# Performance work log

Measured on AMD Instinct MI355X. Metric: run time of the kernel, lower is better.

## Reference

```python
import jax, jax.numpy as jnp
import numpy as np

# __init__ constants
COORS_RANGE = ((-51.2, 51.2), (-51.2, 51.2), (-4.0, 2.4))  # x, y, z ranges
SPATIAL = (512, 512, 64)  # base spatial shape (X, Y, Z)
SCALES = (2, 4, 8, 1)     # scale_list + [1]
N_POINTS = 2_000_000
N_BATCH = 8


def setup_inputs() -> dict:
    key = jax.random.key(0)
    kp, kb = jax.random.split(key)
    lo = jnp.array([r[0] for r in COORS_RANGE], dtype=jnp.float32)
    hi = jnp.array([r[1] for r in COORS_RANGE], dtype=jnp.float32)
    u = jax.random.uniform(kp, (N_POINTS, 3), dtype=jnp.float32)
    points = lo + u * (hi - lo)  # [N,3] xyz inside the voxelization range
    batch_idx = jax.random.randint(kb, (N_POINTS,), 0, N_BATCH).astype(jnp.int64)
    return {"points": points, "batch_idx": batch_idx}


def reference(points, batch_idx):
    """Per scale: quantize xyz to voxel indices, then unique/dedup with inverse and
    counts. Rows [b,x,y,z] are packed into a single int64 key so that a 1-D unique
    (lexicographically equivalent to torch.unique(dim=0)) can be used.
    Returns, for each scale in SCALES: (full_coors [N,4] int64, coors_inv [N] int,
    coors [M,4] int32 in [b,z,y,x] order), flattened into one tuple."""
    b = batch_idx.astype(jnp.int64)
    outs = []
    for scale in SCALES:
        dims = [int(np.ceil(s / scale)) for s in SPATIAL]  # per-scale grid size
        idxs = []
        for i in range(3):
            lo, hi = COORS_RANGE[i]
            # torch .long() truncates toward zero; values are >=0 in range so
            # truncation == floor here.
            idxs.append((dims[i] * (points[:, i] - lo) / (hi - lo)).astype(jnp.int64))
        xidx, yidx, zidx = idxs
        full_coors = jnp.stack([b, xidx, yidx, zidx], axis=-1)  # [N,4]
        sx, sy, sz = dims
        # pack (b,x,y,z) lexicographically into one key
        keys = ((b * sx + xidx) * sy + yidx) * sz + zidx
        unq, unq_inv, unq_cnt = jnp.unique(keys, return_inverse=True, return_counts=True)
        zb = unq % sz
        rem = unq // sz
        yb = rem % sy
        rem = rem // sy
        xb = rem % sx
        bb = rem // sx
        # original reorders unq columns to [b, z, y, x] and casts to int32
        coors = jnp.stack([bb, zb, yb, xb], axis=-1).astype(jnp.int32)
        outs.extend([full_coors, unq_inv.reshape(-1), coors])
    return tuple(outs)
```

## Files before the change

kernel.cpp:

```cpp
#include <hip/hip_runtime.h>
#include <stdint.h>


#define CHUNK 4096
#define NB    1174
#define TOTALW 4808704
#define R_S2 0
#define R_S4 528384
#define R_S8 598016
#define R_S1 610304
#define PAD0 524288
#define PAD1 593920
#define PAD2 606208
#define PAD3 4804608
#define NBUCKET 512
#define BCAP 5120
#define KEYBLOCKS 1024
#define ROUND 2048
#define KPT 8

__device__ __forceinline__ uint32_t cmp2(uint32_t w) {
  w = (w | (w >> 1)) & 0x55555555u;
  w = (w | (w >> 1)) & 0x33333333u;
  w = (w | (w >> 2)) & 0x0F0F0F0Fu;
  w = (w | (w >> 4)) & 0x00FF00FFu;
  w = (w | (w >> 8)) & 0x0000FFFFu;
  return w;
}

__global__ __launch_bounds__(256) void k_key(
    const float* __restrict__ pts, const int* __restrict__ bidx, int n,
    uint32_t* __restrict__ keys,
    uint32_t* __restrict__ bucketCount, uint32_t* __restrict__ bucketData,
    uint32_t* __restrict__ chunkSums) {
  __shared__ uint32_t cnt[NBUCKET], inc[NBUCKET], pos[NBUCKET], gpos[NBUCKET];
  __shared__ uint32_t shs[256];
  __shared__ uint32_t scratch[ROUND];
  int t = threadIdx.x;
  int base = blockIdx.x * ROUND;

  if (blockIdx.x == 0) {
    if (t < 149) chunkSums[t] = 0;
    if (t == 149) chunkSums[1173] = 0;
  }

  cnt[t] = 0; cnt[t + 256] = 0;
  pos[t] = 0; pos[t + 256] = 0;
  __syncthreads();

  uint32_t myKey[KPT];
  int myBk[KPT];
#pragma unroll
  for (int k = 0; k < KPT; k++) {
    int j = base + k * 256 + t;
    myBk[k] = -1;
    if (j < n) {
      float px = pts[3 * j + 0];
      float py = pts[3 * j + 1];
      float pz = pts[3 * j + 2];
      int b = bidx[j];
      int x1 = (int)((512.0f * (px + 51.2f)) / 102.4f);
      int y1 = (int)((512.0f * (py + 51.2f)) / 102.4f);
      int z1 = (int)((64.0f * (pz + 4.0f)) / 6.4f);
      keys[j] = ((uint32_t)b << 27) | ((uint32_t)x1 << 17) | ((uint32_t)y1 << 7) | (uint32_t)z1;
      uint32_t s1k = (uint32_t)(((b * 512 + x1) * 512 + y1) * 64 + z1);
      if (s1k < (1u << 27)) {
        int bk = (int)(s1k >> 18);
        myBk[k] = bk;
        myKey[k] = s1k;
        atomicAdd(&cnt[bk], 1u);
      }
    }
  }
  __syncthreads();

  uint32_t c0 = cnt[2 * t], c1 = cnt[2 * t + 1];
  gpos[2 * t] = c0 ? atomicAdd(&bucketCount[2 * t], c0) : 0u;
  gpos[2 * t + 1] = c1 ? atomicAdd(&bucketCount[2 * t + 1], c1) : 0u;
  uint32_t s = c0 + c1;
  shs[t] = s;
  __syncthreads();
  for (int off = 1; off < 256; off <<= 1) {
    uint32_t add = (t >= off) ? shs[t - off] : 0u;
    __syncthreads();
    shs[t] += add;
    __syncthreads();
  }
  inc[2 * t] = shs[t] - s + c0;
  inc[2 * t + 1] = shs[t];
  __syncthreads();
  uint32_t total = shs[255];

#pragma unroll
  for (int k = 0; k < KPT; k++) {
    if (myBk[k] >= 0) {
      int bk = myBk[k];
      uint32_t slot = inc[bk] - cnt[bk] + atomicAdd(&pos[bk], 1u);
      scratch[slot] = myKey[k];
    }
  }
  __syncthreads();

#pragma unroll
  for (int m = 0; m < KPT; m++) {
    uint32_t p = (uint32_t)(m * 256 + t);
    if (p < total) {
      uint32_t kk = scratch[p];
      int lo = (int)(kk >> 18);
      uint32_t lidx = p - (inc[lo] - cnt[lo]);
      uint32_t g = gpos[lo] + lidx;
      if (g < BCAP) bucketData[(size_t)lo * BCAP + g] = kk;
    }
  }
}

__device__ __forceinline__ uint32_t blockReduce(uint32_t v, uint32_t* shR, int t) {
  shR[t] = v;
  __syncthreads();
  for (int off = 128; off > 0; off >>= 1) {
    if (t < off) shR[t] += shR[t + off];
    __syncthreads();
  }
  uint32_t r = shR[0];
  __syncthreads();
  return r;
}

__global__ __launch_bounds__(256) void k_bucket(
    const uint32_t* __restrict__ bucketCount, const uint32_t* __restrict__ bucketData,
    uint32_t* __restrict__ bitmap, uint32_t* __restrict__ chunkSums) {
  __shared__ uint32_t s1L[8192];
  __shared__ uint32_t s2L[1024];
  __shared__ uint32_t s4L[128];
  __shared__ uint32_t shR[256];
  int bk = blockIdx.x, t = threadIdx.x;

  uint4 z4 = make_uint4(0, 0, 0, 0);
  for (int i = t; i < 2048; i += 256) ((uint4*)s1L)[i] = z4;

  if (bk < 4) {
    const int pads[4] = {PAD0, PAD1, PAD2, PAD3};
    uint4* pz = (uint4*)(bitmap + pads[bk]);
    for (int i = t; i < 1024; i += 256) pz[i] = z4;
  }
  __syncthreads();

  uint32_t c = bucketCount[bk];
  if (c > BCAP) c = BCAP;
  const uint32_t* src = bucketData + (size_t)bk * BCAP;
  for (uint32_t i = t; i < c; i += 256) {
    uint32_t key = src[i];
    uint32_t local = key & 0x3FFFFu;
    atomicOr(&s1L[local >> 5], 1u << (local & 31u));
  }
  __syncthreads();

  uint4* g1 = (uint4*)(bitmap + R_S1 + (size_t)bk * 8192);
  uint32_t pc1a = 0, pc1b = 0;
  for (int i = t; i < 2048; i += 256) {
    uint4 v = ((uint4*)s1L)[i];
    g1[i] = v;
    uint32_t pc = __popc(v.x) + __popc(v.y) + __popc(v.z) + __popc(v.w);
    if (i < 1024) pc1a += pc; else pc1b += pc;
  }

  for (int i = t; i < 1024; i += 256) {
    int x2r = i >> 8, Y2 = i & 255;
    int a = (2 * x2r * 512 + 2 * Y2) * 2;
    int b2 = ((2 * x2r + 1) * 512 + 2 * Y2) * 2;
    uint32_t Ax = s1L[a], Ay = s1L[a + 1], Az = s1L[a + 2], Aw = s1L[a + 3];
    uint32_t Bx = s1L[b2], By = s1L[b2 + 1], Bz = s1L[b2 + 2], Bw = s1L[b2 + 3];
    s2L[i] = cmp2(Ax | Az | Bx | Bz) | (cmp2(Ay | Aw | By | Bw) << 16);
  }
  __syncthreads();
  uint32_t pc2 = 0;
  for (int i = t; i < 1024; i += 256) {
    uint32_t v = s2L[i];
    bitmap[R_S2 + (size_t)bk * 1024 + i] = v;
    pc2 += __popc(v);
  }

  uint32_t pc4 = 0;
  if (t < 128) {
    int x4r = t >> 6, kk = t & 63;
    int a = (2 * x4r) * 256 + 4 * kk;
    int b4 = (2 * x4r + 1) * 256 + 4 * kk;
    uint32_t A0 = s2L[a], A1 = s2L[a + 1], A2 = s2L[a + 2], A3 = s2L[a + 3];
    uint32_t B0 = s2L[b4], B1 = s2L[b4 + 1], B2 = s2L[b4 + 2], B3 = s2L[b4 + 3];
    uint32_t v = cmp2(A0 | A1 | B0 | B1) | (cmp2(A2 | A3 | B2 | B3) << 16);
    s4L[t] = v;
    pc4 = __popc(v);
  }
  __syncthreads();
  if (t < 128) bitmap[R_S4 + (size_t)bk * 128 + t] = s4L[t];

  uint32_t pc8 = 0;
  if (t < 16) {
    uint32_t res = 0;
#pragma unroll
    for (int j = 0; j < 4; j++) {
      uint32_t u = s4L[4 * t + j] | s4L[64 + 4 * t + j];
      u = (u | (u >> 16)) & 0xFFFFu;
      res |= cmp2(u) << (8 * j);
    }
    bitmap[R_S8 + (size_t)bk * 16 + t] = res;
    pc8 = __popc(res);
  }

  uint32_t S1a = blockReduce(pc1a, shR, t);
  uint32_t S1b = blockReduce(pc1b, shR, t);
  uint32_t S2 = blockReduce(pc2, shR, t);
  uint32_t S4 = blockReduce(pc4, shR, t);
  uint32_t S8 = blockReduce(pc8, shR, t);
  if (t == 0) {
    chunkSums[149 + 2 * bk] = S1a;
    chunkSums[150 + 2 * bk] = S1b;
    atomicAdd(&chunkSums[bk >> 2], S2);
    atomicAdd(&chunkSums[129 + (bk >> 5)], S4);
    atomicAdd(&chunkSums[146 + (bk >> 8)], S8);
  }
}

__global__ __launch_bounds__(256) void k_scanB(
    uint32_t* blockSums, long long* devOff, uint32_t* devRank, long long fiveN) {
  __shared__ uint32_t sh[256];
  __shared__ uint32_t shB[3];
  int t = threadIdx.x;
  uint32_t v[8];
  uint32_t s = 0;
#pragma unroll
  for (int k = 0; k < 8; k++) {
    int idx = t * 8 + k;
    uint32_t x = (idx < NB) ? blockSums[idx] : 0u;
    v[k] = x;
    s += x;
  }
  sh[t] = s;
  __syncthreads();
  for (int off = 1; off < 256; off <<= 1) {
    uint32_t add = (t >= off) ? sh[t - off] : 0u;
    __syncthreads();
    sh[t] += add;
    __syncthreads();
  }
  uint32_t run = sh[t] - s;
#pragma unroll
  for (int k = 0; k < 8; k++) {
    int idx = t * 8 + k;
    if (idx < NB) blockSums[idx] = run;
    if (idx == 129) shB[0] = run;
    if (idx == 146) shB[1] = run;
    if (idx == 149) shB[2] = run;
    run += v[k];
  }
  __syncthreads();
  if (t == 0) {
    uint32_t tot = sh[255];
    uint32_t T0 = shB[0];
    uint32_t T1 = shB[1] - shB[0];
    uint32_t T2 = shB[2] - shB[1];
    uint32_t T3 = tot - shB[2];
    devOff[0] = 0;
    devOff[1] = devOff[0] + fiveN + 4LL * T0;
    devOff[2] = devOff[1] + fiveN + 4LL * T1;
    devOff[3] = devOff[2] + fiveN + 4LL * T2;
    devOff[4] = devOff[3] + fiveN + 4LL * T3;
    devRank[0] = 0;
    devRank[1] = shB[0];
    devRank[2] = shB[1];
    devRank[3] = shB[2];
  }
}

__global__ __launch_bounds__(256) void k_pref(
    const uint32_t* __restrict__ bitmap, const uint32_t* __restrict__ blockSums,
    uint2* __restrict__ pairs) {
  __shared__ uint32_t sh[256];
  int t = threadIdx.x;
  size_t w0 = (size_t)blockIdx.x * CHUNK + t * 16;
  const uint4* bp = (const uint4*)(bitmap + w0);
  uint4 words[4];
  uint32_t s = 0;
#pragma unroll
  for (int k = 0; k < 4; k++) {
    uint4 v = bp[k];
    words[k] = v;
    s += __popc(v.x) + __popc(v.y) + __popc(v.z) + __popc(v.w);
  }
  sh[t] = s;
  __syncthreads();
  for (int off = 1; off < 256; off <<= 1) {
    uint32_t add = (t >= off) ? sh[t - off] : 0u;
    __syncthreads();
    sh[t] += add;
    __syncthreads();
  }
  uint32_t run = blockSums[blockIdx.x] + (sh[t] - s);
  uint4* pp = (uint4*)(pairs + w0);
#pragma unroll
  for (int k = 0; k < 4; k++) {
    uint4 o1, o2;
    o1.x = words[k].x; o1.y = run; run += __popc(words[k].x);
    o1.z = words[k].y; o1.w = run; run += __popc(words[k].y);
    o2.x = words[k].z; o2.y = run; run += __popc(words[k].z);
    o2.z = words[k].w; o2.w = run; run += __popc(words[k].w);
    pp[2 * k] = o1;
    pp[2 * k + 1] = o2;
  }
}

template <int LZ, int LYZ, int LB, int MZ, int MY, int MX, int RG, int SCALE_IDX>
__device__ __forceinline__ void uniq_region(
    uint32_t w, uint32_t wd, uint32_t pf, uint32_t rankBase,
    const long long* __restrict__ devOff, int* __restrict__ out, long long fiveN) {
  uint32_t pos = pf - rankBase;
  long long base = devOff[SCALE_IDX] + fiveN;
  uint32_t local = w - (uint32_t)RG;
  while (wd) {
    int bit = __ffs(wd) - 1;
    wd &= wd - 1u;
    uint32_t key = (local << 5) + (uint32_t)bit;
    int z = (int)(key & (uint32_t)MZ);
    int y = (int)((key >> LZ) & (uint32_t)MY);
    int x = (int)((key >> LYZ) & (uint32_t)MX);
    int bb = (int)(key >> LB);
    *(int4*)(out + base + 4LL * pos) = make_int4(bb, z, y, x);
    pos++;
  }
}

__global__ __launch_bounds__(256) void k_out(
    const uint32_t* __restrict__ keys, int n, const uint2* __restrict__ pairs,
    const uint32_t* __restrict__ devRank, const long long* __restrict__ devOff,
    int* __restrict__ out, long long fourN, long long fiveN, int NW) {
  int bid = blockIdx.x;
  int t = threadIdx.x;
  if (bid < 4 * NW) {
    int sec = bid / NW;
    int wb = bid - sec * NW;
    const int SCI[4] = {3, 0, 1, 2};
    const int SX[4] = {256, 128, 64, 512};
    const int SZ[4] = {32, 16, 8, 64};
    const int SH[4] = {1, 2, 3, 0};
    const int RG[4] = {R_S2, R_S4, R_S8, R_S1};
    int i = SCI[sec];
    int sh = SH[i], sx = SX[i], sz = SZ[i], rg = RG[i];
    long long o = devOff[i];
    uint32_t rnk = devRank[i];
#pragma unroll
    for (int half = 0; half < 2; half++) {
      int j = wb * 512 + half * 256 + t;
      if (j >= n) continue;
      uint32_t p = keys[j];
      int b = (int)(p >> 27);
      int x1 = (int)((p >> 17) & 1023u);
      int y1 = (int)((p >> 7) & 1023u);
      int z1 = (int)(p & 127u);
      int xi = x1 >> sh, yi = y1 >> sh, zi = z1 >> sh;
      uint32_t key = (uint32_t)(((b * sx + xi) * sx + yi) * sz + zi);
      uint2 pr = pairs[rg + (key >> 5)];
      *(int4*)(out + o + 4LL * j) = make_int4(b, xi, yi, zi);
      uint32_t inv = pr.y + __popc(pr.x & ((1u << (key & 31u)) - 1u)) - rnk;
      out[o + fourN + j] = (int)inv;
    }
  } else {
    uint32_t w = (uint32_t)(bid - 4 * NW) * 256 + t;
    uint2 pr = pairs[w];
    if (!pr.x) return;
    if (w < R_S4) {
      uniq_region<5, 13, 21, 31, 255, 255, R_S2, 0>(w, pr.x, pr.y, devRank[0], devOff, out, fiveN);
    } else if (w < R_S8) {
      uniq_region<4, 11, 18, 15, 127, 127, R_S4, 1>(w, pr.x, pr.y, devRank[1], devOff, out, fiveN);
    } else if (w < R_S1) {
      uniq_region<3, 9, 15, 7, 63, 63, R_S8, 2>(w, pr.x, pr.y, devRank[2], devOff, out, fiveN);
    } else {
      uniq_region<6, 15, 24, 63, 511, 511, R_S1, 3>(w, pr.x, pr.y, devRank[3], devOff, out, fiveN);
    }
  }
}

extern "C" void kernel_launch(void* const* d_in, const int* in_sizes, int n_in,
                              void* d_out, int out_size, void* d_ws, size_t ws_size,
                              hipStream_t stream) {
  const float* pts = (const float*)d_in[0];
  const int* bidx = (const int*)d_in[1];
  int n = in_sizes[0] / 3;
  int* out = (int*)d_out;

  char* ws = (char*)d_ws;
  long long* devOff = (long long*)ws;
  uint32_t* devRank = (uint32_t*)(ws + 64);
  uint32_t* chunkSums = (uint32_t*)(ws + 256);
  uint32_t* bucketCount = (uint32_t*)(ws + 5120);
  uint32_t* bitmap = (uint32_t*)(ws + 8192);
  uint2* pairs = (uint2*)(ws + 19243008);
  uint32_t* keys = (uint32_t*)(ws + 57712640);
  uint32_t* bucketData = (uint32_t*)(ws + 65712640);

  const long long fourN = 4LL * n, fiveN = 5LL * n;
  const int NW = (n + 511) / 512;

  hipMemsetAsync(bucketCount, 0, NBUCKET * 4, stream);
  hipLaunchKernelGGL(k_key, dim3(KEYBLOCKS), dim3(256), 0, stream,
                     pts, bidx, n, keys, bucketCount, bucketData, chunkSums);
  hipLaunchKernelGGL(k_bucket, dim3(NBUCKET), dim3(256), 0, stream,
                     bucketCount, bucketData, bitmap, chunkSums);
  hipLaunchKernelGGL(k_scanB, dim3(1), dim3(256), 0, stream, chunkSums, devOff, devRank, fiveN);
  hipLaunchKernelGGL(k_pref, dim3(NB), dim3(256), 0, stream, bitmap, chunkSums, pairs);
  hipLaunchKernelGGL(k_out, dim3(4 * NW + TOTALW / 256), dim3(256), 0, stream,
                     keys, n, pairs, devRank, devOff, out, fourN, fiveN, NW);
}
```

Baseline: 426.3 us.

## Fuse scan into bucket kernel via last-block pattern; split scale-1 inverse by batch

New measurement: 434.4 us. Within noise of the previous version (+1.9%).

```diff
diff --git a/kernel.cpp b/kernel.cpp
--- a/kernel.cpp
+++ b/kernel.cpp
@@ -127,12 +127,15 @@
 }
 
 __global__ __launch_bounds__(256) void k_bucket(
-    const uint32_t* __restrict__ bucketCount, const uint32_t* __restrict__ bucketData,
-    uint32_t* __restrict__ bitmap, uint32_t* __restrict__ chunkSums) {
+    uint32_t* __restrict__ bucketCount, const uint32_t* __restrict__ bucketData,
+    uint32_t* __restrict__ bitmap, uint32_t* __restrict__ chunkSums,
+    long long* __restrict__ devOff, uint32_t* __restrict__ devRank, long long fiveN) {
   __shared__ uint32_t s1L[8192];
   __shared__ uint32_t s2L[1024];
   __shared__ uint32_t s4L[128];
   __shared__ uint32_t shR[256];
+  __shared__ uint32_t shB[3];
+  __shared__ uint32_t lastFlag;
   int bk = blockIdx.x, t = threadIdx.x;
 
   uint4 z4 = make_uint4(0, 0, 0, 0);
@@ -219,56 +222,58 @@
     atomicAdd(&chunkSums[129 + (bk >> 5)], S4);
     atomicAdd(&chunkSums[146 + (bk >> 8)], S8);
   }
-}
-
-__global__ __launch_bounds__(256) void k_scanB(
-    uint32_t* blockSums, long long* devOff, uint32_t* devRank, long long fiveN) {
-  __shared__ uint32_t sh[256];
-  __shared__ uint32_t shB[3];
-  int t = threadIdx.x;
-  uint32_t v[8];
-  uint32_t s = 0;
-#pragma unroll
-  for (int k = 0; k < 8; k++) {
-    int idx = t * 8 + k;
-    uint32_t x = (idx < NB) ? blockSums[idx] : 0u;
-    v[k] = x;
-    s += x;
-  }
-  sh[t] = s;
-  __syncthreads();
-  for (int off = 1; off < 256; off <<= 1) {
-    uint32_t add = (t >= off) ? sh[t - off] : 0u;
-    __syncthreads();
-    sh[t] += add;
-    __syncthreads();
-  }
-  uint32_t run = sh[t] - s;
-#pragma unroll
-  for (int k = 0; k < 8; k++) {
-    int idx = t * 8 + k;
-    if (idx < NB) blockSums[idx] = run;
-    if (idx == 129) shB[0] = run;
-    if (idx == 146) shB[1] = run;
-    if (idx == 149) shB[2] = run;
-    run += v[k];
-  }
-  __syncthreads();
+
   if (t == 0) {
-    uint32_t tot = sh[255];
-    uint32_t T0 = shB[0];
-    uint32_t T1 = shB[1] - shB[0];
-    uint32_t T2 = shB[2] - shB[1];
-    uint32_t T3 = tot - shB[2];
-    devOff[0] = 0;
-    devOff[1] = devOff[0] + fiveN + 4LL * T0;
-    devOff[2] = devOff[1] + fiveN + 4LL * T1;
-    devOff[3] = devOff[2] + fiveN + 4LL * T2;
-    devOff[4] = devOff[3] + fiveN + 4LL * T3;
-    devRank[0] = 0;
-    devRank[1] = shB[0];
-    devRank[2] = shB[1];
-    devRank[3] = shB[2];
+    __threadfence();
+    lastFlag = (atomicAdd(&bucketCount[NBUCKET], 1u) == NBUCKET - 1) ? 1u : 0u;
+  }
+  __syncthreads();
+  if (lastFlag) {
+    __threadfence();
+    uint32_t v[8];
+    uint32_t s = 0;
+#pragma unroll
+    for (int k = 0; k < 8; k++) {
+      int idx = t * 8 + k;
+      uint32_t x = (idx < NB) ? chunkSums[idx] : 0u;
+      v[k] = x;
+      s += x;
+    }
+    shR[t] = s;
+    __syncthreads();
+    for (int off = 1; off < 256; off <<= 1) {
+      uint32_t add = (t >= off) ? shR[t - off] : 0u;
+      __syncthreads();
+      shR[t] += add;
+      __syncthreads();
+    }
+    uint32_t run = shR[t] - s;
+#pragma unroll
+    for (int k = 0; k < 8; k++) {
+      int idx = t * 8 + k;
+      if (idx < NB) chunkSums[idx] = run;
+      if (idx == 129) shB[0] = run;
+      if (idx == 146) shB[1] = run;
+      if (idx == 149) shB[2] = run;
+      run += v[k];
+    }
+    __syncthreads();
+    if (t == 0) {
+      uint32_t tot = shR[255];
+      uint32_t T0 = shB[0];
+      uint32_t T1 = shB[1] - shB[0];
+      uint32_t T2 = shB[2] - shB[1];
+      uint32_t T3 = tot - shB[2];
+      devOff[0] = 0;
+      devOff[1] = devOff[0] + fiveN + 4LL * T0;
+      devOff[2] = devOff[1] + fiveN + 4LL * T1;
+      devOff[3] = devOff[2] + fiveN + 4LL * T2;
+      devOff[4] = devOff[3] + fiveN + 4LL * T3;
+      devRank[0] = 0;
+      devRank[1] = shB[0];
+      devRank[2] = shB[1];
+      devRank[3] = shB[2];
+    }
   }
 }
 
@@ -335,15 +340,48 @@
     int* __restrict__ out, long long fourN, long long fiveN, int NW) {
   int bid = blockIdx.x;
   int t = threadIdx.x;
-  if (bid < 4 * NW) {
-    int sec = bid / NW;
-    int wb = bid - sec * NW;
-    const int SCI[4] = {3, 0, 1, 2};
-    const int SX[4] = {256, 128, 64, 512};
-    const int SZ[4] = {32, 16, 8, 64};
-    const int SH[4] = {1, 2, 3, 0};
-    const int RG[4] = {R_S2, R_S4, R_S8, R_S1};
-    int i = SCI[sec];
+  if (bid < 8 * NW) {
+    int r = bid / NW;
+    int wb = bid - r * NW;
+    long long o = devOff[3];
+    uint32_t rnk = devRank[3];
+#pragma unroll
+    for (int half = 0; half < 2; half++) {
+      int j = wb * 512 + half * 256 + t;
+      if (j >= n) continue;
+      uint32_t p = keys[j];
+      int b = (int)(p >> 27);
+      if (b != r) continue;
+      int x1 = (int)((p >> 17) & 1023u);
+      int y1 = (int)((p >> 7) & 1023u);
+      int z1 = (int)(p & 127u);
+      uint32_t key = (uint32_t)(((b * 512 + x1) * 512 + y1) * 64 + z1);
+      uint2 pr = pairs[R_S1 + (key >> 5)];
+      uint32_t inv = pr.y + __popc(pr.x & ((1u << (key & 31u)) - 1u)) - rnk;
+      out[o + fourN + j] = (int)inv;
+    }
+  } else if (bid < 9 * NW) {
+    int wb = bid - 8 * NW;
+    long long o = devOff[3];
+#pragma unroll
+    for (int half = 0; half < 2; half++) {
+      int j = wb * 512 + half * 256 + t;
+      if (j >= n) continue;
+      uint32_t p = keys[j];
+      int b = (int)(p >> 27);
+      int x1 = (int)((p >> 17) & 1023u);
+      int y1 = (int)((p >> 7) & 1023u);
+      int z1 = (int)(p & 127u);
+      *(int4*)(out + o + 4LL * j) = make_int4(b, x1, y1, z1);
+    }
+  } else if (bid < 12 * NW) {
+    int sec = (bid - 9 * NW) / NW;
+    int wb = (bid - 9 * NW) - sec * NW;
+    const int SX[3] = {256, 128, 64};
+    const int SZ[3] = {32, 16, 8};
+    const int SH[3] = {1, 2, 3};
+    const int RG[3] = {R_S2, R_S4, R_S8};
+    int i = sec;
     int sh = SH[i], sx = SX[i], sz = SZ[i], rg = RG[i];
     long long o = devOff[i];
     uint32_t rnk = devRank[i];
@@ -364,7 +402,7 @@
       out[o + fourN + j] = (int)inv;
     }
   } else {
-    uint32_t w = (uint32_t)(bid - 4 * NW) * 256 + t;
+    uint32_t w = (uint32_t)(bid - 12 * NW) * 256 + t;
     uint2 pr = pairs[w];
     if (!pr.x) return;
     if (w < R_S4) {
@@ -400,13 +438,12 @@
   const long long fourN = 4LL * n, fiveN = 5LL * n;
   const int NW = (n + 511) / 512;
 
-  hipMemsetAsync(bucketCount, 0, NBUCKET * 4, stream);
+  hipMemsetAsync(bucketCount, 0, (NBUCKET + 1) * 4, stream);
   hipLaunchKernelGGL(k_key, dim3(KEYBLOCKS), dim3(256), 0, stream,
                      pts, bidx, n, keys, bucketCount, bucketData, chunkSums);
   hipLaunchKernelGGL(k_bucket, dim3(NBUCKET), dim3(256), 0, stream,
-                     bucketCount, bucketData, bitmap, chunkSums);
-  hipLaunchKernelGGL(k_scanB, dim3(1), dim3(256), 0, stream, chunkSums, devOff, devRank, fiveN);
+                     bucketCount, bucketData, bitmap, chunkSums, devOff, devRank, fiveN);
   hipLaunchKernelGGL(k_pref, dim3(NB), dim3(256), 0, stream, bitmap, chunkSums, pairs);
-  hipLaunchKernelGGL(k_out, dim3(4 * NW + TOTALW / 256), dim3(256), 0, stream,
+  hipLaunchKernelGGL(k_out, dim3(12 * NW + TOTALW / 256), dim3(256), 0, stream,
                      keys, n, pairs, devRank, devOff, out, fourN, fiveN, NW);
 }
```

## Fold block-sum scan into last bucket block and vectorize output key loads

Applied to the files above, without the earlier changes.

After: 443.0 us. 3.9% more time.

```diff
diff --git a/kernel.cpp b/kernel.cpp
--- a/kernel.cpp
+++ b/kernel.cpp
@@ -127,12 +127,15 @@
 }
 
 __global__ __launch_bounds__(256) void k_bucket(
-    const uint32_t* __restrict__ bucketCount, const uint32_t* __restrict__ bucketData,
-    uint32_t* __restrict__ bitmap, uint32_t* __restrict__ chunkSums) {
+    uint32_t* __restrict__ bucketCount, const uint32_t* __restrict__ bucketData,
+    uint32_t* __restrict__ bitmap, uint32_t* __restrict__ chunkSums,
+    long long* __restrict__ devOff, uint32_t* __restrict__ devRank, long long fiveN) {
   __shared__ uint32_t s1L[8192];
   __shared__ uint32_t s2L[1024];
   __shared__ uint32_t s4L[128];
   __shared__ uint32_t shR[256];
+  __shared__ uint32_t shB[3];
+  __shared__ uint32_t lastFlag;
   int bk = blockIdx.x, t = threadIdx.x;
 
   uint4 z4 = make_uint4(0, 0, 0, 0);
@@ -219,56 +222,58 @@
     atomicAdd(&chunkSums[129 + (bk >> 5)], S4);
     atomicAdd(&chunkSums[146 + (bk >> 8)], S8);
   }
-}
-
-__global__ __launch_bounds__(256) void k_scanB(
-    uint32_t* blockSums, long long* devOff, uint32_t* devRank, long long fiveN) {
-  __shared__ uint32_t sh[256];
-  __shared__ uint32_t shB[3];
-  int t = threadIdx.x;
-  uint32_t v[8];
-  uint32_t s = 0;
-#pragma unroll
-  for (int k = 0; k < 8; k++) {
-    int idx = t * 8 + k;
-    uint32_t x = (idx < NB) ? blockSums[idx] : 0u;
-    v[k] = x;
-    s += x;
-  }
-  sh[t] = s;
-  __syncthreads();
-  for (int off = 1; off < 256; off <<= 1) {
-    uint32_t add = (t >= off) ? sh[t - off] : 0u;
-    __syncthreads();
-    sh[t] += add;
-    __syncthreads();
-  }
-  uint32_t run = sh[t] - s;
-#pragma unroll
-  for (int k = 0; k < 8; k++) {
-    int idx = t * 8 + k;
-    if (idx < NB) blockSums[idx] = run;
-    if (idx == 129) shB[0] = run;
-    if (idx == 146) shB[1] = run;
-    if (idx == 149) shB[2] = run;
-    run += v[k];
-  }
-  __syncthreads();
+
   if (t == 0) {
-    uint32_t tot = sh[255];
-    uint32_t T0 = shB[0];
-    uint32_t T1 = shB[1] - shB[0];
-    uint32_t T2 = shB[2] - shB[1];
-    uint32_t T3 = tot - shB[2];
-    devOff[0] = 0;
-    devOff[1] = devOff[0] + fiveN + 4LL * T0;
-    devOff[2] = devOff[1] + fiveN + 4LL * T1;
-    devOff[3] = devOff[2] + fiveN + 4LL * T2;
-    devOff[4] = devOff[3] + fiveN + 4LL * T3;
-    devRank[0] = 0;
-    devRank[1] = shB[0];
-    devRank[2] = shB[1];
-    devRank[3] = shB[2];
+    __threadfence();
+    lastFlag = (atomicAdd(&bucketCount[NBUCKET], 1u) == NBUCKET - 1) ? 1u : 0u;
+  }
+  __syncthreads();
+  if (lastFlag) {
+    __threadfence();
+    uint32_t v[8];
+    uint32_t s = 0;
+#pragma unroll
+    for (int k = 0; k < 8; k++) {
+      int idx = t * 8 + k;
+      uint32_t x = (idx < NB) ? chunkSums[idx] : 0u;
+      v[k] = x;
+      s += x;
+    }
+    shR[t] = s;
+    __syncthreads();
+    for (int off = 1; off < 256; off <<= 1) {
+      uint32_t add = (t >= off) ? shR[t - off] : 0u;
+      __syncthreads();
+      shR[t] += add;
+      __syncthreads();
+    }
+    uint32_t run = shR[t] - s;
+#pragma unroll
+    for (int k = 0; k < 8; k++) {
+      int idx = t * 8 + k;
+      if (idx < NB) chunkSums[idx] = run;
+      if (idx == 129) shB[0] = run;
+      if (idx == 146) shB[1] = run;
+      if (idx == 149) shB[2] = run;
+      run += v[k];
+    }
+    __syncthreads();
+    if (t == 0) {
+      uint32_t tot = shR[255];
+      uint32_t T0 = shB[0];
+      uint32_t T1 = shB[1] - shB[0];
+      uint32_t T2 = shB[2] - shB[1];
+      uint32_t T3 = tot - shB[2];
+      devOff[0] = 0;
+      devOff[1] = devOff[0] + fiveN + 4LL * T0;
+      devOff[2] = devOff[1] + fiveN + 4LL * T1;
+      devOff[3] = devOff[2] + fiveN + 4LL * T2;
+      devOff[4] = devOff[3] + fiveN + 4LL * T3;
+      devRank[0] = 0;
+      devRank[1] = shB[0];
+      devRank[2] = shB[1];
+      devRank[3] = shB[2];
+    }
   }
 }
 
@@ -329,15 +334,31 @@
   }
 }
 
+__device__ __forceinline__ void write_point(
+    uint32_t p, int j, int sh, int sx, int sz, int rg,
+    long long o, uint32_t rnk, const uint2* __restrict__ pairs,
+    int* __restrict__ out, long long fourN) {
+  int b = (int)(p >> 27);
+  int x1 = (int)((p >> 17) & 1023u);
+  int y1 = (int)((p >> 7) & 1023u);
+  int z1 = (int)(p & 127u);
+  int xi = x1 >> sh, yi = y1 >> sh, zi = z1 >> sh;
+  uint32_t key = (uint32_t)(((b * sx + xi) * sx + yi) * sz + zi);
+  uint2 pr = pairs[rg + (key >> 5)];
+  *(int4*)(out + o + 4LL * j) = make_int4(b, xi, yi, zi);
+  uint32_t inv = pr.y + __popc(pr.x & ((1u << (key & 31u)) - 1u)) - rnk;
+  out[o + fourN + j] = (int)inv;
+}
+
 __global__ __launch_bounds__(256) void k_out(
     const uint32_t* __restrict__ keys, int n, const uint2* __restrict__ pairs,
     const uint32_t* __restrict__ devRank, const long long* __restrict__ devOff,
-    int* __restrict__ out, long long fourN, long long fiveN, int NW) {
+    int* __restrict__ out, long long fourN, long long fiveN, int NW4) {
   int bid = blockIdx.x;
   int t = threadIdx.x;
-  if (bid < 4 * NW) {
-    int sec = bid / NW;
-    int wb = bid - sec * NW;
+  if (bid < 4 * NW4) {
+    int sec = bid / NW4;
+    int wb = bid - sec * NW4;
     const int SCI[4] = {3, 0, 1, 2};
     const int SX[4] = {256, 128, 64, 512};
     const int SZ[4] = {32, 16, 8, 64};
@@ -347,24 +368,19 @@
     int sh = SH[i], sx = SX[i], sz = SZ[i], rg = RG[i];
     long long o = devOff[i];
     uint32_t rnk = devRank[i];
-#pragma unroll
-    for (int half = 0; half < 2; half++) {
-      int j = wb * 512 + half * 256 + t;
-      if (j >= n) continue;
-      uint32_t p = keys[j];
-      int b = (int)(p >> 27);
-      int x1 = (int)((p >> 17) & 1023u);
-      int y1 = (int)((p >> 7) & 1023u);
-      int z1 = (int)(p & 127u);
-      int xi = x1 >> sh, yi = y1 >> sh, zi = z1 >> sh;
-      uint32_t key = (uint32_t)(((b * sx + xi) * sx + yi) * sz + zi);
-      uint2 pr = pairs[rg + (key >> 5)];
-      *(int4*)(out + o + 4LL * j) = make_int4(b, xi, yi, zi);
-      uint32_t inv = pr.y + __popc(pr.x & ((1u << (key & 31u)) - 1u)) - rnk;
-      out[o + fourN + j] = (int)inv;
+    int j0 = wb * 1024 + 4 * t;
+    if (j0 + 3 < n) {
+      uint4 kv = *(const uint4*)(keys + j0);
+      write_point(kv.x, j0 + 0, sh, sx, sz, rg, o, rnk, pairs, out, fourN);
+      write_point(kv.y, j0 + 1, sh, sx, sz, rg, o, rnk, pairs, out, fourN);
+      write_point(kv.z, j0 + 2, sh, sx, sz, rg, o, rnk, pairs, out, fourN);
+      write_point(kv.w, j0 + 3, sh, sx, sz, rg, o, rnk, pairs, out, fourN);
+    } else {
+      for (int j = j0; j < n; j++)
+        write_point(keys[j], j, sh, sx, sz, rg, o, rnk, pairs, out, fourN);
     }
   } else {
-    uint32_t w = (uint32_t)(bid - 4 * NW) * 256 + t;
+    uint32_t w = (uint32_t)(bid - 4 * NW4) * 256 + t;
     uint2 pr = pairs[w];
     if (!pr.x) return;
     if (w < R_S4) {
@@ -398,15 +414,14 @@
   uint32_t* bucketData = (uint32_t*)(ws + 65712640);
 
   const long long fourN = 4LL * n, fiveN = 5LL * n;
-  const int NW = (n + 511) / 512;
-
-  hipMemsetAsync(bucketCount, 0, NBUCKET * 4, stream);
+  const int NW4 = (n + 1023) / 1024;
+
+  hipMemsetAsync(bucketCount, 0, (NBUCKET + 1) * 4, stream);
   hipLaunchKernelGGL(k_key, dim3(KEYBLOCKS), dim3(256), 0, stream,
                      pts, bidx, n, keys, bucketCount, bucketData, chunkSums);
   hipLaunchKernelGGL(k_bucket, dim3(NBUCKET), dim3(256), 0, stream,
-                     bucketCount, bucketData, bitmap, chunkSums);
-  hipLaunchKernelGGL(k_scanB, dim3(1), dim3(256), 0, stream, chunkSums, devOff, devRank, fiveN);
+                     bucketCount, bucketData, bitmap, chunkSums, devOff, devRank, fiveN);
   hipLaunchKernelGGL(k_pref, dim3(NB), dim3(256), 0, stream, bitmap, chunkSums, pairs);
-  hipLaunchKernelGGL(k_out, dim3(4 * NW + TOTALW / 256), dim3(256), 0, stream,
-                     keys, n, pairs, devRank, devOff, out, fourN, fiveN, NW);
-}
+  hipLaunchKernelGGL(k_out, dim3(4 * NW4 + TOTALW / 256), dim3(256), 0, stream,
+                     keys, n, pairs, devRank, devOff, out, fourN, fiveN, NW4);
+}
```

## Build scale-1 bitmap prefix pairs in bucket kernel and shrink prefix pass

Applied to the files above, without the earlier changes.

Result: no change. 427.4 us (+0.2%).

```diff
diff --git a/kernel.cpp b/kernel.cpp
--- a/kernel.cpp
+++ b/kernel.cpp
@@ -18,6 +18,7 @@
 #define KEYBLOCKS 1024
 #define ROUND 2048
 #define KPT 8
+#define NB_SMALL 149
 
 __device__ __forceinline__ uint32_t cmp2(uint32_t w) {
   w = (w | (w >> 1)) & 0x55555555u;
@@ -128,7 +129,8 @@
 
 __global__ __launch_bounds__(256) void k_bucket(
     const uint32_t* __restrict__ bucketCount, const uint32_t* __restrict__ bucketData,
-    uint32_t* __restrict__ bitmap, uint32_t* __restrict__ chunkSums) {
+    uint32_t* __restrict__ bitmap, uint32_t* __restrict__ chunkSums,
+    uint2* __restrict__ pairs) {
   __shared__ uint32_t s1L[8192];
   __shared__ uint32_t s2L[1024];
   __shared__ uint32_t s4L[128];
@@ -138,10 +140,13 @@
   uint4 z4 = make_uint4(0, 0, 0, 0);
   for (int i = t; i < 2048; i += 256) ((uint4*)s1L)[i] = z4;
 
-  if (bk < 4) {
-    const int pads[4] = {PAD0, PAD1, PAD2, PAD3};
+  if (bk < 3) {
+    const int pads[3] = {PAD0, PAD1, PAD2};
     uint4* pz = (uint4*)(bitmap + pads[bk]);
     for (int i = t; i < 1024; i += 256) pz[i] = z4;
+  } else if (bk == 3) {
+    uint4* pz = (uint4*)(pairs + PAD3);
+    for (int i = t; i < 2048; i += 256) pz[i] = z4;
   }
   __syncthreads();
 
@@ -155,13 +160,38 @@
   }
   __syncthreads();
 
-  uint4* g1 = (uint4*)(bitmap + R_S1 + (size_t)bk * 8192);
-  uint32_t pc1a = 0, pc1b = 0;
-  for (int i = t; i < 2048; i += 256) {
-    uint4 v = ((uint4*)s1L)[i];
-    g1[i] = v;
-    uint32_t pc = __popc(v.x) + __popc(v.y) + __popc(v.z) + __popc(v.w);
-    if (i < 1024) pc1a += pc; else pc1b += pc;
+  uint32_t wsum = 0;
+#pragma unroll
+  for (int m = 0; m < 8; m++) {
+    uint4 v = ((uint4*)s1L)[8 * t + m];
+    wsum += __popc(v.x) + __popc(v.y) + __popc(v.z) + __popc(v.w);
+  }
+  shR[t] = wsum;
+  __syncthreads();
+  for (int off = 1; off < 256; off <<= 1) {
+    uint32_t add = (t >= off) ? shR[t - off] : 0u;
+    __syncthreads();
+    shR[t] += add;
+    __syncthreads();
+  }
+  uint32_t S1a = shR[127];
+  uint32_t S1b = shR[255] - S1a;
+  uint32_t run = shR[t] - wsum;
+  if (t >= 128) run -= S1a;
+  __syncthreads();
+  {
+    uint4* pb = (uint4*)(pairs + (R_S1 + (size_t)bk * 8192));
+#pragma unroll
+    for (int m = 0; m < 8; m++) {
+      uint4 v = ((uint4*)s1L)[8 * t + m];
+      uint32_t r0 = run;               uint32_t p0 = __popc(v.x);
+      uint32_t r1 = r0 + p0;           uint32_t p1 = __popc(v.y);
+      uint32_t r2 = r1 + p1;           uint32_t p2 = __popc(v.z);
+      uint32_t r3 = r2 + p2;           run = r3 + __popc(v.w);
+      int q = (32 * t + 4 * m) >> 1;
+      pb[q + 0] = make_uint4(v.x, r0, v.y, r1);
+      pb[q + 1] = make_uint4(v.z, r2, v.w, r3);
+    }
   }
 
   for (int i = t; i < 1024; i += 256) {
@@ -207,8 +237,6 @@
     pc8 = __popc(res);
   }
 
-  uint32_t S1a = blockReduce(pc1a, shR, t);
-  uint32_t S1b = blockReduce(pc1b, shR, t);
   uint32_t S2 = blockReduce(pc2, shR, t);
   uint32_t S4 = blockReduce(pc4, shR, t);
   uint32_t S8 = blockReduce(pc8, shR, t);
@@ -332,36 +360,57 @@
 __global__ __launch_bounds__(256) void k_out(
     const uint32_t* __restrict__ keys, int n, const uint2* __restrict__ pairs,
     const uint32_t* __restrict__ devRank, const long long* __restrict__ devOff,
-    int* __restrict__ out, long long fourN, long long fiveN, int NW) {
+    const uint32_t* __restrict__ cs, int* __restrict__ out,
+    long long fourN, long long fiveN, int NW) {
   int bid = blockIdx.x;
   int t = threadIdx.x;
   if (bid < 4 * NW) {
     int sec = bid / NW;
     int wb = bid - sec * NW;
-    const int SCI[4] = {3, 0, 1, 2};
-    const int SX[4] = {256, 128, 64, 512};
-    const int SZ[4] = {32, 16, 8, 64};
-    const int SH[4] = {1, 2, 3, 0};
-    const int RG[4] = {R_S2, R_S4, R_S8, R_S1};
-    int i = SCI[sec];
-    int sh = SH[i], sx = SX[i], sz = SZ[i], rg = RG[i];
-    long long o = devOff[i];
-    uint32_t rnk = devRank[i];
-#pragma unroll
-    for (int half = 0; half < 2; half++) {
-      int j = wb * 512 + half * 256 + t;
-      if (j >= n) continue;
-      uint32_t p = keys[j];
-      int b = (int)(p >> 27);
-      int x1 = (int)((p >> 17) & 1023u);
-      int y1 = (int)((p >> 7) & 1023u);
-      int z1 = (int)(p & 127u);
-      int xi = x1 >> sh, yi = y1 >> sh, zi = z1 >> sh;
-      uint32_t key = (uint32_t)(((b * sx + xi) * sx + yi) * sz + zi);
-      uint2 pr = pairs[rg + (key >> 5)];
-      *(int4*)(out + o + 4LL * j) = make_int4(b, xi, yi, zi);
-      uint32_t inv = pr.y + __popc(pr.x & ((1u << (key & 31u)) - 1u)) - rnk;
-      out[o + fourN + j] = (int)inv;
+    if (sec == 0) {
+      long long o = devOff[3];
+      uint32_t rnk = devRank[3];
+#pragma unroll
+      for (int half = 0; half < 2; half++) {
+        int j = wb * 512 + half * 256 + t;
+        if (j >= n) continue;
+        uint32_t p = keys[j];
+        int b = (int)(p >> 27);
+        int x1 = (int)((p >> 17) & 1023u);
+        int y1 = (int)((p >> 7) & 1023u);
+        int z1 = (int)(p & 127u);
+        uint32_t key = (uint32_t)(((b * 512 + x1) * 512 + y1) * 64 + z1);
+        uint2 pr = pairs[R_S1 + (key >> 5)];
+        *(int4*)(out + o + 4LL * j) = make_int4(b, x1, y1, z1);
+        uint32_t inv = cs[149 + (key >> 17)] + pr.y +
+                       __popc(pr.x & ((1u << (key & 31u)) - 1u)) - rnk;
+        out[o + fourN + j] = (int)inv;
+      }
+    } else {
+      int i = sec - 1;
+      const int SX[3] = {256, 128, 64};
+      const int SZ[3] = {32, 16, 8};
+      const int SH[3] = {1, 2, 3};
+      const int RG[3] = {R_S2, R_S4, R_S8};
+      int sh = SH[i], sx = SX[i], sz = SZ[i], rg = RG[i];
+      long long o = devOff[i];
+      uint32_t rnk = devRank[i];
+#pragma unroll
+      for (int half = 0; half < 2; half++) {
+        int j = wb * 512 + half * 256 + t;
+        if (j >= n) continue;
+        uint32_t p = keys[j];
+        int b = (int)(p >> 27);
+        int x1 = (int)((p >> 17) & 1023u);
+        int y1 = (int)((p >> 7) & 1023u);
+        int z1 = (int)(p & 127u);
+        int xi = x1 >> sh, yi = y1 >> sh, zi = z1 >> sh;
+        uint32_t key = (uint32_t)(((b * sx + xi) * sx + yi) * sz + zi);
+        uint2 pr = pairs[rg + (key >> 5)];
+        *(int4*)(out + o + 4LL * j) = make_int4(b, xi, yi, zi);
+        uint32_t inv = pr.y + __popc(pr.x & ((1u << (key & 31u)) - 1u)) - rnk;
+        out[o + fourN + j] = (int)inv;
+      }
     }
   } else {
     uint32_t w = (uint32_t)(bid - 4 * NW) * 256 + t;
@@ -374,7 +423,8 @@
     } else if (w < R_S1) {
       uniq_region<3, 9, 15, 7, 63, 63, R_S8, 2>(w, pr.x, pr.y, devRank[2], devOff, out, fiveN);
     } else {
-      uniq_region<6, 15, 24, 63, 511, 511, R_S1, 3>(w, pr.x, pr.y, devRank[3], devOff, out, fiveN);
+      uniq_region<6, 15, 24, 63, 511, 511, R_S1, 3>(
+          w, pr.x, pr.y + cs[w >> 12], devRank[3], devOff, out, fiveN);
     }
   }
 }
@@ -404,9 +454,9 @@
   hipLaunchKernelGGL(k_key, dim3(KEYBLOCKS), dim3(256), 0, stream,
                      pts, bidx, n, keys, bucketCount, bucketData, chunkSums);
   hipLaunchKernelGGL(k_bucket, dim3(NBUCKET), dim3(256), 0, stream,
-                     bucketCount, bucketData, bitmap, chunkSums);
+                     bucketCount, bucketData, bitmap, chunkSums, pairs);
   hipLaunchKernelGGL(k_scanB, dim3(1), dim3(256), 0, stream, chunkSums, devOff, devRank, fiveN);
-  hipLaunchKernelGGL(k_pref, dim3(NB), dim3(256), 0, stream, bitmap, chunkSums, pairs);
+  hipLaunchKernelGGL(k_pref, dim3(NB_SMALL), dim3(256), 0, stream, bitmap, chunkSums, pairs);
   hipLaunchKernelGGL(k_out, dim3(4 * NW + TOTALW / 256), dim3(256), 0, stream,
-                     keys, n, pairs, devRank, devOff, out, fourN, fiveN, NW);
-}
+                     keys, n, pairs, devRank, devOff, chunkSums, out, fourN, fiveN, NW);
+}
```
